# Optimization experiments

Measured on AMD Instinct MI355X. Metric: run time of the kernel, lower is better.

The kernel has to match this reference:

```python
import jax, jax.numpy as jnp
import numpy as np

EPS = 1e-20
K = 3        # kernel_size
STRIDE = 2
PAD = 1
DIL = 1
B, C, O, H, W = 4, 32, 32, 256, 256
HO = (H + 2 * PAD - DIL * (K - 1) - 1) // STRIDE + 1  # 128
WO = (W + 2 * PAD - DIL * (K - 1) - 1) // STRIDE + 1  # 128


def kernel_channels(x):
    """Unfold-like gather: [B,C,H,W] -> [B,C,K*K,HO,WO] (zero-padded)."""
    xp = jnp.pad(x, ((0, 0), (0, 0), (PAD, PAD), (PAD, PAD)))
    patches = [
        xp[:, :, i * DIL : i * DIL + (HO - 1) * STRIDE + 1 : STRIDE,
              j * DIL : j * DIL + (WO - 1) * STRIDE + 1 : STRIDE]
        for i in range(K) for j in range(K)
    ]
    return jnp.stack(patches, axis=2)


def setup_inputs() -> dict:
    key = jax.random.key(0)
    ks = jax.random.split(key, 11)
    return {
        "d":   jax.random.normal(ks[0], (B, C, H, W), jnp.float32),
        "cd":  jax.random.uniform(ks[1], (B, C, H, W), jnp.float32),
        "s":   jax.random.uniform(ks[2], (B, C, H, W), jnp.float32),
        "cs":  jax.random.uniform(ks[3], (B, C, H, W), jnp.float32),
        "gx":  jax.random.normal(ks[4], (B, C, H, W), jnp.float32),
        "cgx": jax.random.uniform(ks[5], (B, C, H, W), jnp.float32),
        "s_prod_roll": jax.random.uniform(ks[6], (B, C, K * K, HO, WO), jnp.float32),
        # learned parameters (raw; softplus applied in forward via EnforcePos)
        "w_prop":         jax.random.normal(ks[7], (1, C, 1, 1), jnp.float32) * 0.5,
        "spatial_weight": jax.random.normal(ks[8], (C, 1, K * K, 1, 1), jnp.float32) * 0.5,
        "channel_weight": jax.random.normal(ks[9], (O, C, 1, 1), jnp.float32) * 0.5,
        "bias":           jax.random.normal(ks[10], (1, O, 1, 1), jnp.float32) * 0.01,
    }


def reference(d, cd, s, cs, gx, cgx, s_prod_roll,
              w_prop, spatial_weight, channel_weight, bias):
    # EnforcePos: positive reparametrization of the weights
    wp = jax.nn.softplus(w_prop)                          # [1,C,1,1]
    sw = jax.nn.softplus(spatial_weight)[:, 0, :, 0, 0]   # [C,K*K]
    cw = jax.nn.softplus(channel_weight)[:, :, 0, 0]      # [O,C]

    # width-dim shift/pad (exactly matches F.pad(x[...,: -1], (0,1)) etc.)
    pad_r = lambda x: jnp.pad(x[:, :, :, :-1], ((0, 0), (0, 0), (0, 0), (0, 1)))
    pad_l = lambda x: jnp.pad(x[:, :, :, 1:],  ((0, 0), (0, 0), (0, 0), (1, 0)))
    d_left,  cd_left,  s_left  = pad_r(d), pad_r(cd), pad_r(s)
    d_right, cd_right, s_right = pad_l(d), pad_l(cd), pad_l(s)

    cgx_from_ds = s * s_left * s_right * cd_left * cd_right
    height = (cd_left * d_left + cd_right * d_right) / (cd_left + cd_right + EPS)
    gx_from_ds = (d_right - d_left) / 2 / (height + EPS)

    gx = (wp * cgx * gx + cgx_from_ds * gx_from_ds) / (wp * cgx + cgx_from_ds + EPS)
    cgx = (wp * cgx + cgx_from_ds) / (wp + 1.0)

    gx_roll = kernel_channels(gx)        # [B,C,K*K,HO,WO]
    cgx_roll = kernel_channels(cgx)
    cgx_prop = cgx_roll * s_prod_roll

    # spatial stage: grouped conv3d over kernel-channel dim == per-channel 9-tap reduce
    nom = jnp.einsum('bckhw,ck->bchw', cgx_prop * gx_roll, sw)
    den = jnp.einsum('bckhw,ck->bchw', cgx_prop, sw)
    gx_sp = nom / (den + EPS)
    cgx_sp = den / (jnp.sum(sw) + EPS)

    # channel stage: 1x1 conv2d (groups=1)
    nom2 = jnp.einsum('bchw,oc->bohw', cgx_sp * gx_sp, cw)
    den2 = jnp.einsum('bchw,oc->bohw', cgx_sp, cw)
    gx_out = nom2 / (den2 + EPS) + bias
    cgx_out = den2 / (jnp.sum(cw) + EPS)

    # devalue_pooled_confidence=True
    return gx_out * STRIDE, cgx_out / (STRIDE * STRIDE)
```

## Files before the change

### kernel.cpp

```cpp
#include <hip/hip_runtime.h>
#include <math.h>

#define EPSF 1e-20f
#define Bv 4
#define Cv 32
#define Ov 32
#define Hv 256
#define Wv 256
#define HOv 128
#define WOv 128
#define NPIX (HOv * WOv)
#define HALF_OUT (Bv * Ov * NPIX)

__device__ __forceinline__ float softplus_f(float x) {
    return fmaxf(x, 0.0f) + log1pf(__expf(-fabsf(x)));
}
__device__ __forceinline__ float frcp(float x) {
    return __builtin_amdgcn_rcpf(x);
}

__device__ __forceinline__ float4 gload4(const float* p) {
    float4 r;
    asm volatile("global_load_dwordx4 %0, %1, off" : "=v"(r) : "v"(p));
    return r;
}
__device__ __forceinline__ float2 gload2(const float* p) {
    float2 r;
    asm volatile("global_load_dwordx2 %0, %1, off" : "=v"(r) : "v"(p));
    return r;
}
__device__ __forceinline__ void vm_drain() {
    asm volatile("s_waitcnt vmcnt(0)" ::: "memory");
    __builtin_amdgcn_sched_barrier(0);
}

#define WS_BUF_OFF 2048
#define WS_NEEDED (WS_BUF_OFF * 4 + (size_t)Bv * Cv * NPIX * 8)

__global__ void prep_kernel(const float* __restrict__ wp_raw,
                            const float* __restrict__ sw_raw,
                            const float* __restrict__ cw_raw,
                            float* __restrict__ ws) {
    __shared__ float red_sw[256];
    __shared__ float red_cw[256];
    const int t = threadIdx.x;
    float acc_sw = 0.f, acc_cw = 0.f;
    if (t < 32) ws[t] = softplus_f(wp_raw[t]);
    for (int i = t; i < 288; i += 256) {
        float v = softplus_f(sw_raw[i]);
        ws[32 + i] = v;
        acc_sw += v;
    }
    for (int i = t; i < 1024; i += 256) {
        float v = softplus_f(cw_raw[i]);
        ws[320 + i] = v;
        acc_cw += v;
    }
    red_sw[t] = acc_sw;
    red_cw[t] = acc_cw;
    __syncthreads();
    for (int st = 128; st > 0; st >>= 1) {
        if (t < st) { red_sw[t] += red_sw[t + st]; red_cw[t] += red_cw[t + st]; }
        __syncthreads();
    }
    if (t == 0) {
        ws[1344] = 1.0f / (red_sw[0] + EPSF);
        ws[1345] = 1.0f / (red_cw[0] + EPSF);
    }
}

__global__ __launch_bounds__(256, 2)
void k1_spatial(const float* __restrict__ d,  const float* __restrict__ cd,
                const float* __restrict__ s,  const float* __restrict__ gx,
                const float* __restrict__ cgx, const float* __restrict__ sprod,
                const float* __restrict__ ws, float2* __restrict__ buf) {
    const int t  = threadIdx.x;
    const int l  = t & 63;
    const int q  = t >> 6;
    const int ho = blockIdx.x * 4 + q;
    const int z  = blockIdx.y;
    const int c  = z & 31;

    const float wpc = ws[c];
    const float inv_wp1 = frcp(wpc + 1.0f);
    const float inv_sumsw = ws[1344];
    const float* sw_c = ws + 32 + c * 9;

    const int ibase = z * (Hv * Wv);
    const int h_top = 2 * ho - 1;
    const bool row0_ok = (h_top >= 0);
    const int col = 4 * l;

    int gaddr[3];
    gaddr[0] = ibase + (row0_ok ? h_top : 0) * Wv + col;
    gaddr[1] = ibase + (h_top + 1) * Wv + col;
    gaddr[2] = ibase + (h_top + 2) * Wv + col;

    float4 Dv[3], Cd[3], Sv[3], Gv[3], Cg[3];
#pragma unroll
    for (int r = 0; r < 3; ++r) {
        Dv[r] = gload4(d   + gaddr[r]);
        Cd[r] = gload4(cd  + gaddr[r]);
        Sv[r] = gload4(s   + gaddr[r]);
        Gv[r] = gload4(gx  + gaddr[r]);
        Cg[r] = gload4(cgx + gaddr[r]);
    }
    const int sp0 = (z * 9 * HOv + ho) * WOv + 2 * l;
    float2 sp[9];
#pragma unroll
    for (int k = 0; k < 9; ++k)
        sp[k] = gload2(sprod + sp0 + k * NPIX);

    vm_drain();

    float nom0 = 0.f, den0 = 0.f, nom1 = 0.f, den1 = 0.f;
#pragma unroll
    for (int r = 0; r < 3; ++r) {
        const bool vrow = (r > 0) || row0_ok;
        const float* Df = (const float*)&Dv[r];
        const float* CDf = (const float*)&Cd[r];
        const float* Sf = (const float*)&Sv[r];
        const float* Gf = (const float*)&Gv[r];
        const float* Cf = (const float*)&Cg[r];
        float gn[4], cn[4];
#pragma unroll
        for (int e = 0; e < 4; ++e) {
            const int w = col + e;
            const bool mL = (w != Wv - 1);
            const bool mR = (w != 0);
            const float dV = Df[e], cdV = CDf[e], sV = Sf[e];
            const float dL  = mL ? dV  : 0.f;
            const float cdL = mL ? cdV : 0.f;
            const float sL  = mL ? sV  : 0.f;
            const float dR  = mR ? dV  : 0.f;
            const float cdR = mR ? cdV : 0.f;
            const float sR  = mR ? sV  : 0.f;
            const float cgx_ds = sV * sL * sR * cdL * cdR;
            const float height = (cdL * dL + cdR * dR) * frcp(cdL + cdR + EPSF);
            const float gx_ds  = (dR - dL) * 0.5f * frcp(height + EPSF);
            const float a = wpc * Cf[e];
            const float g_ = (a * Gf[e] + cgx_ds * gx_ds) * frcp(a + cgx_ds + EPSF);
            const float c_ = (a + cgx_ds) * inv_wp1;
            gn[e] = vrow ? g_ : 0.f;
            cn[e] = vrow ? c_ : 0.f;
        }
        float ge = __shfl_up(gn[3], 1, 64);
        float ce = __shfl_up(cn[3], 1, 64);
        ge = l ? ge : 0.f;
        ce = l ? ce : 0.f;
        const float sw0 = sw_c[3 * r + 0];
        const float sw1 = sw_c[3 * r + 1];
        const float sw2 = sw_c[3 * r + 2];
        float cp;
        cp = ce    * sp[3 * r + 0].x * sw0; den0 += cp; nom0 = fmaf(cp, ge,    nom0);
        cp = cn[0] * sp[3 * r + 1].x * sw1; den0 += cp; nom0 = fmaf(cp, gn[0], nom0);
        cp = cn[1] * sp[3 * r + 2].x * sw2; den0 += cp; nom0 = fmaf(cp, gn[1], nom0);
        cp = cn[1] * sp[3 * r + 0].y * sw0; den1 += cp; nom1 = fmaf(cp, gn[1], nom1);
        cp = cn[2] * sp[3 * r + 1].y * sw1; den1 += cp; nom1 = fmaf(cp, gn[2], nom1);
        cp = cn[3] * sp[3 * r + 2].y * sw2; den1 += cp; nom1 = fmaf(cp, gn[3], nom1);
    }
    const float gx0 = nom0 * frcp(den0 + EPSF);
    const float cg0 = den0 * inv_sumsw;
    const float gx1 = nom1 * frcp(den1 + EPSF);
    const float cg1 = den1 * inv_sumsw;
    float4 ov = {cg0 * gx0, cg0, cg1 * gx1, cg1};
    *(float4*)(buf + (size_t)z * NPIX + ho * WOv + 2 * l) = ov;
}

__global__ __launch_bounds__(256, 2)
void k2_channel(const float2* __restrict__ buf, const float* __restrict__ ws,
                const float* __restrict__ bias, float* __restrict__ out) {
    const int pg  = blockIdx.x * 256 + threadIdx.x;
    const int b   = pg >> 14;
    const int pp  = pg & (NPIX - 1);
    const int grp = blockIdx.y;
    const float* cw_t = ws + 320;
    const float inv_sumcw = ws[1345];

    const int cbase = b * Cv * NPIX + pp;

    float2 v[Cv];
#pragma unroll
    for (int cc = 0; cc < Cv; ++cc)
        v[cc] = gload2((const float*)(buf + cbase + cc * NPIX));

    vm_drain();

    float nom2[16], den2[16];
#pragma unroll
    for (int i = 0; i < 16; ++i) { nom2[i] = 0.f; den2[i] = 0.f; }

#pragma unroll
    for (int cc = 0; cc < Cv; ++cc) {
#pragma unroll
        for (int oi = 0; oi < 16; ++oi) {
            const float w_ = cw_t[(grp * 16 + oi) * Cv + cc];
            nom2[oi] = fmaf(v[cc].x, w_, nom2[oi]);
            den2[oi] = fmaf(v[cc].y, w_, den2[oi]);
        }
    }
#pragma unroll
    for (int oi = 0; oi < 16; ++oi) {
        const int o = grp * 16 + oi;
        const int p = (b * Ov + o) * NPIX + pp;
        const float dn = den2[oi];
        const float g  = nom2[oi] * frcp(dn + EPSF) + bias[o];
        out[p]            = g * 2.0f;
        out[HALF_OUT + p] = dn * inv_sumcw * 0.25f;
    }
}

#define TH 4
#define TW 32
#define IH 9
#define IW 65
#define IWP 66
#define NTILE (IH * IW)

__global__ __launch_bounds__(128)
void main_kernel(const float* __restrict__ d,  const float* __restrict__ cd,
                 const float* __restrict__ s,  const float* __restrict__ gx,
                 const float* __restrict__ cgx, const float* __restrict__ sprod,
                 const float* __restrict__ bias, const float* __restrict__ ws,
                 float* __restrict__ out) {
    __shared__ float lgx[IH][IWP];
    __shared__ float lcgx[IH][IWP];
    const int t    = threadIdx.x;
    const int wo_l = t & 31;
    const int ho_l = t >> 5;
    const int wo0  = blockIdx.x * TW;
    const int ho0  = blockIdx.y * TH;
    const int b    = blockIdx.z;
    const int ho   = ho0 + ho_l;
    const int wo   = wo0 + wo_l;
    const float* sw_t = ws + 32;
    const float* cw_t = ws + 320;
    const float inv_sumsw = ws[1344];
    const float inv_sumcw = ws[1345];
    float nom2[Ov], den2[Ov];
#pragma unroll
    for (int o = 0; o < Ov; ++o) { nom2[o] = 0.f; den2[o] = 0.f; }
    const int h_base = 2 * ho0 - 1;
    const int w_base = 2 * wo0 - 1;
    for (int c = 0; c < Cv; ++c) {
        const float wpc = ws[c];
        const float inv_wp1 = frcp(wpc + 1.0f);
        const int ibase = (b * Cv + c) * (Hv * Wv);
        for (int idx = t; idx < NTILE; idx += 128) {
            const int r  = idx / IW;
            const int cc = idx - r * IW;
            const int h  = h_base + r;
            const int w  = w_base + cc;
            float gxn = 0.f, cgxn = 0.f;
            if ((unsigned)h < (unsigned)Hv && (unsigned)w < (unsigned)Wv) {
                const int p = ibase + h * Wv + w;
                const float dv = d[p], cdv = cd[p], sv = s[p];
                const float gxv = gx[p], cgxv = cgx[p];
                const bool mLb = (w != Wv - 1);
                const bool mRb = (w != 0);
                const float dL = mLb ? dv : 0.f, cdL = mLb ? cdv : 0.f, sL = mLb ? sv : 0.f;
                const float dR = mRb ? dv : 0.f, cdR = mRb ? cdv : 0.f, sR = mRb ? sv : 0.f;
                const float cgx_ds = sv * sL * sR * cdL * cdR;
                const float height = (cdL * dL + cdR * dR) * frcp(cdL + cdR + EPSF);
                const float gx_ds  = (dR - dL) * 0.5f * frcp(height + EPSF);
                const float a = wpc * cgxv;
                gxn  = (a * gxv + cgx_ds * gx_ds) * frcp(a + cgx_ds + EPSF);
                cgxn = (a + cgx_ds) * inv_wp1;
            }
            lgx[r][cc]  = gxn;
            lcgx[r][cc] = cgxn;
        }
        __syncthreads();
        const int spb = ((b * Cv + c) * 9 * HOv + ho) * WOv + wo;
        float nom = 0.f, den = 0.f;
#pragma unroll
        for (int k = 0; k < 9; ++k) {
            const int ki = k / 3;
            const int kj = k - ki * 3;
            const float gxr  = lgx[2 * ho_l + ki][2 * wo_l + kj];
            const float cgxr = lcgx[2 * ho_l + ki][2 * wo_l + kj];
            const float spv  = sprod[spb + k * NPIX];
            const float cp   = cgxr * spv * sw_t[c * 9 + k];
            den += cp;
            nom = fmaf(cp, gxr, nom);
        }
        const float gx_sp  = nom * frcp(den + EPSF);
        const float cgx_sp = den * inv_sumsw;
        const float t1 = cgx_sp * gx_sp;
#pragma unroll
        for (int o = 0; o < Ov; ++o) {
            const float w_ = cw_t[o * Cv + c];
            nom2[o] = fmaf(t1, w_, nom2[o]);
            den2[o] = fmaf(cgx_sp, w_, den2[o]);
        }
        __syncthreads();
    }
#pragma unroll
    for (int o = 0; o < Ov; ++o) {
        const int p = ((b * Ov + o) * HOv + ho) * WOv + wo;
        const float dn = den2[o];
        const float g  = nom2[o] * frcp(dn + EPSF) + bias[o];
        out[p]            = g * 2.0f;
        out[HALF_OUT + p] = dn * inv_sumcw * 0.25f;
    }
}

extern "C" void kernel_launch(void* const* d_in, const int* in_sizes, int n_in,
                              void* d_out, int out_size, void* d_ws, size_t ws_size,
                              hipStream_t stream) {
    const float* d_ptr    = (const float*)d_in[0];
    const float* cd_ptr   = (const float*)d_in[1];
    const float* s_ptr    = (const float*)d_in[2];
    const float* gx_ptr   = (const float*)d_in[4];
    const float* cgx_ptr  = (const float*)d_in[5];
    const float* sp_ptr   = (const float*)d_in[6];
    const float* wp_ptr   = (const float*)d_in[7];
    const float* sw_ptr   = (const float*)d_in[8];
    const float* cw_ptr   = (const float*)d_in[9];
    const float* bias_ptr = (const float*)d_in[10];
    float* out = (float*)d_out;
    float* ws  = (float*)d_ws;

    prep_kernel<<<1, 256, 0, stream>>>(wp_ptr, sw_ptr, cw_ptr, ws);

    if (ws_size >= WS_NEEDED) {
        float2* buf = (float2*)(ws + WS_BUF_OFF);
        dim3 g1(HOv / 4, Bv * Cv, 1);
        k1_spatial<<<g1, 256, 0, stream>>>(d_ptr, cd_ptr, s_ptr, gx_ptr, cgx_ptr,
                                           sp_ptr, ws, buf);
        dim3 g2((Bv * NPIX) / 256, 2, 1);
        k2_channel<<<g2, 256, 0, stream>>>(buf, ws, bias_ptr, out);
    } else {
        dim3 grid(WOv / TW, HOv / TH, Bv);
        main_kernel<<<grid, 128, 0, stream>>>(d_ptr, cd_ptr, s_ptr, gx_ptr, cgx_ptr,
                                              sp_ptr, bias_ptr, ws, out);
    }
}
```

Measured before the change: 276.7 us.

## Compute two output rows per thread, remap blocks per XCD, merge channel groups

```diff
diff --git a/kernel.cpp b/kernel.cpp
--- a/kernel.cpp
+++ b/kernel.cpp
@@ -69,7 +69,7 @@
     }
 }
 
-__global__ __launch_bounds__(256, 2)
+__global__ __launch_bounds__(256)
 void k1_spatial(const float* __restrict__ d,  const float* __restrict__ cd,
                 const float* __restrict__ s,  const float* __restrict__ gx,
                 const float* __restrict__ cgx, const float* __restrict__ sprod,
@@ -77,9 +77,13 @@
     const int t  = threadIdx.x;
     const int l  = t & 63;
     const int q  = t >> 6;
-    const int ho = blockIdx.x * 4 + q;
-    const int z  = blockIdx.y;
-    const int c  = z & 31;
+    const int f    = blockIdx.x;
+    const int xcd  = f & 7;
+    const int k_   = f >> 3;
+    const int z    = xcd * 16 + (k_ >> 4);
+    const int hop  = (k_ & 15) * 4 + q;
+    const int ho0  = hop * 2;
+    const int c    = z & 31;
 
     const float wpc = ws[c];
     const float inv_wp1 = frcp(wpc + 1.0f);
@@ -87,42 +91,42 @@
     const float* sw_c = ws + 32 + c * 9;
 
     const int ibase = z * (Hv * Wv);
-    const int h_top = 2 * ho - 1;
+    const int h_top = 2 * ho0 - 1;
     const bool row0_ok = (h_top >= 0);
     const int col = 4 * l;
 
-    int gaddr[3];
-    gaddr[0] = ibase + (row0_ok ? h_top : 0) * Wv + col;
-    gaddr[1] = ibase + (h_top + 1) * Wv + col;
-    gaddr[2] = ibase + (h_top + 2) * Wv + col;
-
-    float4 Dv[3], Cd[3], Sv[3], Gv[3], Cg[3];
-#pragma unroll
-    for (int r = 0; r < 3; ++r) {
-        Dv[r] = gload4(d   + gaddr[r]);
-        Cd[r] = gload4(cd  + gaddr[r]);
-        Sv[r] = gload4(s   + gaddr[r]);
-        Gv[r] = gload4(gx  + gaddr[r]);
-        Cg[r] = gload4(cgx + gaddr[r]);
-    }
-    const int sp0 = (z * 9 * HOv + ho) * WOv + 2 * l;
-    float2 sp[9];
-#pragma unroll
-    for (int k = 0; k < 9; ++k)
-        sp[k] = gload2(sprod + sp0 + k * NPIX);
+    int ga[5];
+    ga[0] = ibase + (row0_ok ? h_top : 0) * Wv + col;
+#pragma unroll
+    for (int r = 1; r < 5; ++r) ga[r] = ibase + (h_top + r) * Wv + col;
+
+    float4 Dv[5], Cd[5], Sv[5], Gv[5], Cg[5];
+#pragma unroll
+    for (int r = 0; r < 5; ++r) {
+        Dv[r] = gload4(d   + ga[r]);
+        Cd[r] = gload4(cd  + ga[r]);
+        Sv[r] = gload4(s   + ga[r]);
+        Gv[r] = gload4(gx  + ga[r]);
+        Cg[r] = gload4(cgx + ga[r]);
+    }
+    const int sp0 = (z * 9 * HOv + ho0) * WOv + 2 * l;
+    float2 spA[9], spB[9];
+#pragma unroll
+    for (int k = 0; k < 9; ++k) spA[k] = gload2(sprod + sp0 + k * NPIX);
+#pragma unroll
+    for (int k = 0; k < 9; ++k) spB[k] = gload2(sprod + sp0 + WOv + k * NPIX);
 
     vm_drain();
 
-    float nom0 = 0.f, den0 = 0.f, nom1 = 0.f, den1 = 0.f;
-#pragma unroll
-    for (int r = 0; r < 3; ++r) {
+    float gn[5][4], cn[5][4];
+#pragma unroll
+    for (int r = 0; r < 5; ++r) {
         const bool vrow = (r > 0) || row0_ok;
-        const float* Df = (const float*)&Dv[r];
+        const float* Df  = (const float*)&Dv[r];
         const float* CDf = (const float*)&Cd[r];
-        const float* Sf = (const float*)&Sv[r];
-        const float* Gf = (const float*)&Gv[r];
-        const float* Cf = (const float*)&Cg[r];
-        float gn[4], cn[4];
+        const float* Sf  = (const float*)&Sv[r];
+        const float* Gf  = (const float*)&Gv[r];
+        const float* Cf  = (const float*)&Cg[r];
 #pragma unroll
         for (int e = 0; e < 4; ++e) {
             const int w = col + e;
@@ -141,39 +145,58 @@
             const float a = wpc * Cf[e];
             const float g_ = (a * Gf[e] + cgx_ds * gx_ds) * frcp(a + cgx_ds + EPSF);
             const float c_ = (a + cgx_ds) * inv_wp1;
-            gn[e] = vrow ? g_ : 0.f;
-            cn[e] = vrow ? c_ : 0.f;
-        }
-        float ge = __shfl_up(gn[3], 1, 64);
-        float ce = __shfl_up(cn[3], 1, 64);
-        ge = l ? ge : 0.f;
-        ce = l ? ce : 0.f;
-        const float sw0 = sw_c[3 * r + 0];
-        const float sw1 = sw_c[3 * r + 1];
-        const float sw2 = sw_c[3 * r + 2];
+            gn[r][e] = vrow ? g_ : 0.f;
+            cn[r][e] = vrow ? c_ : 0.f;
+        }
+    }
+    float ge[5], ce[5];
+#pragma unroll
+    for (int r = 0; r < 5; ++r) {
+        float g2 = __shfl_up(gn[r][3], 1, 64);
+        float c2 = __shfl_up(cn[r][3], 1, 64);
+        ge[r] = l ? g2 : 0.f;
+        ce[r] = l ? c2 : 0.f;
+    }
+
+    float n00 = 0.f, d00 = 0.f, n01 = 0.f, d01 = 0.f;
+    float n10 = 0.f, d10 = 0.f, n11 = 0.f, d11 = 0.f;
+#pragma unroll
+    for (int kr = 0; kr < 3; ++kr) {
+        const float sw0 = sw_c[3 * kr + 0];
+        const float sw1 = sw_c[3 * kr + 1];
+        const float sw2 = sw_c[3 * kr + 2];
         float cp;
-        cp = ce    * sp[3 * r + 0].x * sw0; den0 += cp; nom0 = fmaf(cp, ge,    nom0);
-        cp = cn[0] * sp[3 * r + 1].x * sw1; den0 += cp; nom0 = fmaf(cp, gn[0], nom0);
-        cp = cn[1] * sp[3 * r + 2].x * sw2; den0 += cp; nom0 = fmaf(cp, gn[1], nom0);
-        cp = cn[1] * sp[3 * r + 0].y * sw0; den1 += cp; nom1 = fmaf(cp, gn[1], nom1);
-        cp = cn[2] * sp[3 * r + 1].y * sw1; den1 += cp; nom1 = fmaf(cp, gn[2], nom1);
-        cp = cn[3] * sp[3 * r + 2].y * sw2; den1 += cp; nom1 = fmaf(cp, gn[3], nom1);
-    }
-    const float gx0 = nom0 * frcp(den0 + EPSF);
-    const float cg0 = den0 * inv_sumsw;
-    const float gx1 = nom1 * frcp(den1 + EPSF);
-    const float cg1 = den1 * inv_sumsw;
-    float4 ov = {cg0 * gx0, cg0, cg1 * gx1, cg1};
-    *(float4*)(buf + (size_t)z * NPIX + ho * WOv + 2 * l) = ov;
-}
-
-__global__ __launch_bounds__(256, 2)
+        cp = ce[kr]    * spA[3 * kr + 0].x * sw0; d00 += cp; n00 = fmaf(cp, ge[kr],    n00);
+        cp = cn[kr][0] * spA[3 * kr + 1].x * sw1; d00 += cp; n00 = fmaf(cp, gn[kr][0], n00);
+        cp = cn[kr][1] * spA[3 * kr + 2].x * sw2; d00 += cp; n00 = fmaf(cp, gn[kr][1], n00);
+        cp = cn[kr][1] * spA[3 * kr + 0].y * sw0; d01 += cp; n01 = fmaf(cp, gn[kr][1], n01);
+        cp = cn[kr][2] * spA[3 * kr + 1].y * sw1; d01 += cp; n01 = fmaf(cp, gn[kr][2], n01);
+        cp = cn[kr][3] * spA[3 * kr + 2].y * sw2; d01 += cp; n01 = fmaf(cp, gn[kr][3], n01);
+        const int r2 = kr + 2;
+        cp = ce[r2]    * spB[3 * kr + 0].x * sw0; d10 += cp; n10 = fmaf(cp, ge[r2],    n10);
+        cp = cn[r2][0] * spB[3 * kr + 1].x * sw1; d10 += cp; n10 = fmaf(cp, gn[r2][0], n10);
+        cp = cn[r2][1] * spB[3 * kr + 2].x * sw2; d10 += cp; n10 = fmaf(cp, gn[r2][1], n10);
+        cp = cn[r2][1] * spB[3 * kr + 0].y * sw0; d11 += cp; n11 = fmaf(cp, gn[r2][1], n11);
+        cp = cn[r2][2] * spB[3 * kr + 1].y * sw1; d11 += cp; n11 = fmaf(cp, gn[r2][2], n11);
+        cp = cn[r2][3] * spB[3 * kr + 2].y * sw2; d11 += cp; n11 = fmaf(cp, gn[r2][3], n11);
+    }
+    const float gA0 = n00 * frcp(d00 + EPSF), cA0 = d00 * inv_sumsw;
+    const float gA1 = n01 * frcp(d01 + EPSF), cA1 = d01 * inv_sumsw;
+    const float gB0 = n10 * frcp(d10 + EPSF), cB0 = d10 * inv_sumsw;
+    const float gB1 = n11 * frcp(d11 + EPSF), cB1 = d11 * inv_sumsw;
+    float4 o0 = {cA0 * gA0, cA0, cA1 * gA1, cA1};
+    float4 o1 = {cB0 * gB0, cB0, cB1 * gB1, cB1};
+    float2* bp = buf + (size_t)z * NPIX + ho0 * WOv + 2 * l;
+    *(float4*)bp         = o0;
+    *(float4*)(bp + WOv) = o1;
+}
+
+__global__ __launch_bounds__(256)
 void k2_channel(const float2* __restrict__ buf, const float* __restrict__ ws,
                 const float* __restrict__ bias, float* __restrict__ out) {
     const int pg  = blockIdx.x * 256 + threadIdx.x;
     const int b   = pg >> 14;
     const int pp  = pg & (NPIX - 1);
-    const int grp = blockIdx.y;
     const float* cw_t = ws + 320;
     const float inv_sumcw = ws[1345];
 
@@ -186,25 +209,24 @@
 
     vm_drain();
 
-    float nom2[16], den2[16];
-#pragma unroll
-    for (int i = 0; i < 16; ++i) { nom2[i] = 0.f; den2[i] = 0.f; }
+    float nom2[Ov], den2[Ov];
+#pragma unroll
+    for (int i = 0; i < Ov; ++i) { nom2[i] = 0.f; den2[i] = 0.f; }
 
 #pragma unroll
     for (int cc = 0; cc < Cv; ++cc) {
 #pragma unroll
-        for (int oi = 0; oi < 16; ++oi) {
-            const float w_ = cw_t[(grp * 16 + oi) * Cv + cc];
+        for (int oi = 0; oi < Ov; ++oi) {
+            const float w_ = cw_t[oi * Cv + cc];
             nom2[oi] = fmaf(v[cc].x, w_, nom2[oi]);
             den2[oi] = fmaf(v[cc].y, w_, den2[oi]);
         }
     }
 #pragma unroll
-    for (int oi = 0; oi < 16; ++oi) {
-        const int o = grp * 16 + oi;
-        const int p = (b * Ov + o) * NPIX + pp;
+    for (int oi = 0; oi < Ov; ++oi) {
+        const int p = (b * Ov + oi) * NPIX + pp;
         const float dn = den2[oi];
-        const float g  = nom2[oi] * frcp(dn + EPSF) + bias[o];
+        const float g  = nom2[oi] * frcp(dn + EPSF) + bias[oi];
         out[p]            = g * 2.0f;
         out[HALF_OUT + p] = dn * inv_sumcw * 0.25f;
     }
@@ -325,11 +347,9 @@
 
     if (ws_size >= WS_NEEDED) {
         float2* buf = (float2*)(ws + WS_BUF_OFF);
-        dim3 g1(HOv / 4, Bv * Cv, 1);
-        k1_spatial<<<g1, 256, 0, stream>>>(d_ptr, cd_ptr, s_ptr, gx_ptr, cgx_ptr,
-                                           sp_ptr, ws, buf);
-        dim3 g2((Bv * NPIX) / 256, 2, 1);
-        k2_channel<<<g2, 256, 0, stream>>>(buf, ws, bias_ptr, out);
+        k1_spatial<<<2048, 256, 0, stream>>>(d_ptr, cd_ptr, s_ptr, gx_ptr, cgx_ptr,
+                                             sp_ptr, ws, buf);
+        k2_channel<<<(Bv * NPIX) / 256, 256, 0, stream>>>(buf, ws, bias_ptr, out);
     } else {
         dim3 grid(WOv / TW, HOv / TH, Bv);
         main_kernel<<<grid, 128, 0, stream>>>(d_ptr, cd_ptr, s_ptr, gx_ptr, cgx_ptr,
```

Result: slower. 288.0 us (+4.1%).

## Stage overlapping input rows in LDS to share pre-stage across output rows

Applied to the files above, without the earlier changes.

```diff
diff --git a/kernel.cpp b/kernel.cpp
--- a/kernel.cpp
+++ b/kernel.cpp
@@ -74,11 +74,16 @@
                 const float* __restrict__ s,  const float* __restrict__ gx,
                 const float* __restrict__ cgx, const float* __restrict__ sprod,
                 const float* __restrict__ ws, float2* __restrict__ buf) {
+    __shared__ float lds[16128];
+    float* inL = lds;
+    float* gaL = lds + 11520;
+    float* caL = lds + 13824;
+
     const int t  = threadIdx.x;
     const int l  = t & 63;
     const int q  = t >> 6;
-    const int ho = blockIdx.x * 4 + q;
-    const int z  = blockIdx.y;
+    const int z  = blockIdx.x >> 5;
+    const int rt = blockIdx.x & 31;
     const int c  = z & 31;
 
     const float wpc = ws[c];
@@ -86,25 +91,26 @@
     const float inv_sumsw = ws[1344];
     const float* sw_c = ws + 32 + c * 9;
 
-    const int ibase = z * (Hv * Wv);
-    const int h_top = 2 * ho - 1;
-    const bool row0_ok = (h_top >= 0);
-    const int col = 4 * l;
-
-    int gaddr[3];
-    gaddr[0] = ibase + (row0_ok ? h_top : 0) * Wv + col;
-    gaddr[1] = ibase + (h_top + 1) * Wv + col;
-    gaddr[2] = ibase + (h_top + 2) * Wv + col;
-
-    float4 Dv[3], Cd[3], Sv[3], Gv[3], Cg[3];
-#pragma unroll
-    for (int r = 0; r < 3; ++r) {
-        Dv[r] = gload4(d   + gaddr[r]);
-        Cd[r] = gload4(cd  + gaddr[r]);
-        Sv[r] = gload4(s   + gaddr[r]);
-        Gv[r] = gload4(gx  + gaddr[r]);
-        Cg[r] = gload4(cgx + gaddr[r]);
-    }
+    const int ho0     = rt * 4;
+    const int h_top   = 2 * ho0 - 1;
+    const bool top    = (rt == 0);
+    const int h_start = top ? 0 : h_top;
+    const int nf4     = top ? 512 : 576;
+    const int dof     = top ? 256 : 0;
+    const int gbase   = z * (Hv * Wv) + h_start * Wv;
+
+    float4 st[5][3];
+#pragma unroll
+    for (int a = 0; a < 5; ++a) {
+        const float* gp = (a == 0) ? d : (a == 1) ? cd : (a == 2) ? s
+                        : (a == 3) ? gx : cgx;
+#pragma unroll
+        for (int k = 0; k < 3; ++k) {
+            const int o = t + k * 256;
+            if (o < nf4) st[a][k] = gload4(gp + gbase + 4 * o);
+        }
+    }
+    const int ho  = ho0 + q;
     const int sp0 = (z * 9 * HOv + ho) * WOv + 2 * l;
     float2 sp[9];
 #pragma unroll
@@ -113,56 +119,71 @@
 
     vm_drain();
 
-    float nom0 = 0.f, den0 = 0.f, nom1 = 0.f, den1 = 0.f;
-#pragma unroll
-    for (int r = 0; r < 3; ++r) {
-        const bool vrow = (r > 0) || row0_ok;
-        const float* Df = (const float*)&Dv[r];
-        const float* CDf = (const float*)&Cd[r];
-        const float* Sf = (const float*)&Sv[r];
-        const float* Gf = (const float*)&Gv[r];
-        const float* Cf = (const float*)&Cg[r];
-        float gn[4], cn[4];
-#pragma unroll
-        for (int e = 0; e < 4; ++e) {
-            const int w = col + e;
-            const bool mL = (w != Wv - 1);
-            const bool mR = (w != 0);
-            const float dV = Df[e], cdV = CDf[e], sV = Sf[e];
-            const float dL  = mL ? dV  : 0.f;
-            const float cdL = mL ? cdV : 0.f;
-            const float sL  = mL ? sV  : 0.f;
-            const float dR  = mR ? dV  : 0.f;
-            const float cdR = mR ? cdV : 0.f;
-            const float sR  = mR ? sV  : 0.f;
-            const float cgx_ds = sV * sL * sR * cdL * cdR;
-            const float height = (cdL * dL + cdR * dR) * frcp(cdL + cdR + EPSF);
-            const float gx_ds  = (dR - dL) * 0.5f * frcp(height + EPSF);
-            const float a = wpc * Cf[e];
-            const float g_ = (a * Gf[e] + cgx_ds * gx_ds) * frcp(a + cgx_ds + EPSF);
-            const float c_ = (a + cgx_ds) * inv_wp1;
-            gn[e] = vrow ? g_ : 0.f;
-            cn[e] = vrow ? c_ : 0.f;
-        }
-        float ge = __shfl_up(gn[3], 1, 64);
-        float ce = __shfl_up(cn[3], 1, 64);
-        ge = l ? ge : 0.f;
-        ce = l ? ce : 0.f;
-        const float sw0 = sw_c[3 * r + 0];
-        const float sw1 = sw_c[3 * r + 1];
-        const float sw2 = sw_c[3 * r + 2];
+#pragma unroll
+    for (int a = 0; a < 5; ++a) {
+#pragma unroll
+        for (int k = 0; k < 3; ++k) {
+            const int o = t + k * 256;
+            if (o < nf4)
+                *(float4*)(inL + a * 2304 + dof + 4 * o) = st[a][k];
+        }
+    }
+    __syncthreads();
+
+#pragma unroll
+    for (int j = 0; j < 9; ++j) {
+        const int o = j * 256 + t;
+        const float dV  = inL[0 * 2304 + o];
+        const float cdV = inL[1 * 2304 + o];
+        const float sV  = inL[2 * 2304 + o];
+        const float gV  = inL[3 * 2304 + o];
+        const float cV  = inL[4 * 2304 + o];
+        const bool mL = (t != Wv - 1);
+        const bool mR = (t != 0);
+        const float dL  = mL ? dV  : 0.f;
+        const float cdL = mL ? cdV : 0.f;
+        const float sL  = mL ? sV  : 0.f;
+        const float dR  = mR ? dV  : 0.f;
+        const float cdR = mR ? cdV : 0.f;
+        const float sR  = mR ? sV  : 0.f;
+        const float cgx_ds = sV * sL * sR * cdL * cdR;
+        const float height = (cdL * dL + cdR * dR) * frcp(cdL + cdR + EPSF);
+        const float gx_ds  = (dR - dL) * 0.5f * frcp(height + EPSF);
+        const float a_ = wpc * cV;
+        const float g_ = (a_ * gV + cgx_ds * gx_ds) * frcp(a_ + cgx_ds + EPSF);
+        const float c_ = (a_ + cgx_ds) * inv_wp1;
+        const bool vrow = (j > 0) || !top;
+        gaL[o] = vrow ? g_ : 0.f;
+        caL[o] = vrow ? c_ : 0.f;
+    }
+    __syncthreads();
+
+    float n0 = 0.f, d0 = 0.f, n1 = 0.f, d1 = 0.f;
+#pragma unroll
+    for (int ki = 0; ki < 3; ++ki) {
+        const int ro = (2 * q + ki) * 256;
+        const float4 g4 = *(const float4*)(gaL + ro + 4 * l);
+        const float4 c4 = *(const float4*)(caL + ro + 4 * l);
+        const int eo = ro + (l ? 4 * l - 1 : 0);
+        float geL = gaL[eo];
+        float ceL = caL[eo];
+        geL = l ? geL : 0.f;
+        ceL = l ? ceL : 0.f;
+        const float sw0 = sw_c[3 * ki + 0];
+        const float sw1 = sw_c[3 * ki + 1];
+        const float sw2 = sw_c[3 * ki + 2];
         float cp;
-        cp = ce    * sp[3 * r + 0].x * sw0; den0 += cp; nom0 = fmaf(cp, ge,    nom0);
-        cp = cn[0] * sp[3 * r + 1].x * sw1; den0 += cp; nom0 = fmaf(cp, gn[0], nom0);
-        cp = cn[1] * sp[3 * r + 2].x * sw2; den0 += cp; nom0 = fmaf(cp, gn[1], nom0);
-        cp = cn[1] * sp[3 * r + 0].y * sw0; den1 += cp; nom1 = fmaf(cp, gn[1], nom1);
-        cp = cn[2] * sp[3 * r + 1].y * sw1; den1 += cp; nom1 = fmaf(cp, gn[2], nom1);
-        cp = cn[3] * sp[3 * r + 2].y * sw2; den1 += cp; nom1 = fmaf(cp, gn[3], nom1);
-    }
-    const float gx0 = nom0 * frcp(den0 + EPSF);
-    const float cg0 = den0 * inv_sumsw;
-    const float gx1 = nom1 * frcp(den1 + EPSF);
-    const float cg1 = den1 * inv_sumsw;
+        cp = ceL  * sp[3 * ki + 0].x * sw0; d0 += cp; n0 = fmaf(cp, geL,  n0);
+        cp = c4.x * sp[3 * ki + 1].x * sw1; d0 += cp; n0 = fmaf(cp, g4.x, n0);
+        cp = c4.y * sp[3 * ki + 2].x * sw2; d0 += cp; n0 = fmaf(cp, g4.y, n0);
+        cp = c4.y * sp[3 * ki + 0].y * sw0; d1 += cp; n1 = fmaf(cp, g4.y, n1);
+        cp = c4.z * sp[3 * ki + 1].y * sw1; d1 += cp; n1 = fmaf(cp, g4.z, n1);
+        cp = c4.w * sp[3 * ki + 2].y * sw2; d1 += cp; n1 = fmaf(cp, g4.w, n1);
+    }
+    const float gx0 = n0 * frcp(d0 + EPSF);
+    const float cg0 = d0 * inv_sumsw;
+    const float gx1 = n1 * frcp(d1 + EPSF);
+    const float cg1 = d1 * inv_sumsw;
     float4 ov = {cg0 * gx0, cg0, cg1 * gx1, cg1};
     *(float4*)(buf + (size_t)z * NPIX + ho * WOv + 2 * l) = ov;
 }
@@ -325,9 +346,8 @@
 
     if (ws_size >= WS_NEEDED) {
         float2* buf = (float2*)(ws + WS_BUF_OFF);
-        dim3 g1(HOv / 4, Bv * Cv, 1);
-        k1_spatial<<<g1, 256, 0, stream>>>(d_ptr, cd_ptr, s_ptr, gx_ptr, cgx_ptr,
-                                           sp_ptr, ws, buf);
+        k1_spatial<<<4096, 256, 0, stream>>>(d_ptr, cd_ptr, s_ptr, gx_ptr, cgx_ptr,
+                                             sp_ptr, ws, buf);
         dim3 g2((Bv * NPIX) / 256, 2, 1);
         k2_channel<<<g2, 256, 0, stream>>>(buf, ws, bias_ptr, out);
     } else {
```

Measured after the change: 273.6 us. About the same (-1.1%).
